# Optimization experiments

Measured on AMD Instinct MI355X. Metric: run time of the kernel, lower is better.

## Reference

```python
import jax, jax.numpy as jnp
import numpy as np

B, C, H, W = 16, 3, 1024, 1024
DENSITY = 0.015
SIGMA = 1.5
K = 5  # blur kernel size
N_FLAKES = int(H * W * DENSITY)  # 15728


def setup_inputs() -> dict:
    key = jax.random.key(0)
    kx, ky, kxs, kr = jax.random.split(key, 4)
    x = jax.random.uniform(kx, (B, C, H, W), dtype=jnp.float32)
    ys = jax.random.randint(ky, (B, N_FLAKES), 0, H, dtype=jnp.int32)
    xs = jax.random.randint(kxs, (B, N_FLAKES), 0, W, dtype=jnp.int32)
    rs = jax.random.randint(kr, (B, N_FLAKES), 1, 4, dtype=jnp.int32)  # radius in {1,2,3}
    return {"x": x, "ys": ys, "xs": xs, "rs": rs}


def reference(x, ys, xs, rs):
    Bb, Cc, Hh, Ww = x.shape
    # --- vectorized flake stamping (replaces per-flake Python loop) ---
    # Each flake writes a (2r+1)x(2r+1) square of 0.95, clipped to image bounds.
    # Max radius is 3 -> enumerate the 7x7 = 49 candidate offsets per flake.
    off = jnp.arange(-3, 4)
    dyg, dxg = jnp.meshgrid(off, off, indexing="ij")
    dy = dyg.reshape(-1)  # [49]
    dx = dxg.reshape(-1)  # [49]
    r = rs[..., None]  # [B, N, 1]
    valid = (jnp.abs(dy) <= r) & (jnp.abs(dx) <= r)  # [B, N, 49]
    # Clamping out-of-bounds coords to the border is equivalent to torch's
    # slice-clipping because the written value is a constant (0.95) and the
    # border pixel is already covered by an in-range offset. Invalid offsets
    # (|d| > r) are redirected to the flake center, which is always stamped.
    yy = jnp.where(valid, jnp.clip(ys[..., None] + dy, 0, Hh - 1), ys[..., None])
    xx = jnp.where(valid, jnp.clip(xs[..., None] + dx, 0, Ww - 1), xs[..., None])
    b = jnp.arange(Bb)[:, None, None]  # [B,1,1]
    out = x.at[b, :, yy, xx].set(0.95)  # stamp all channels

    # --- depthwise 5x5 gaussian blur ---
    coords = jnp.arange(K, dtype=jnp.float32) - K // 2
    g = jnp.exp(-(coords ** 2) / (2.0 * SIGMA ** 2))
    g = g / g.sum()
    kern = jnp.outer(g, g).astype(x.dtype)[None, None]  # [1,1,5,5]
    kern = jnp.broadcast_to(kern, (Cc, 1, K, K))  # depthwise: O=C, I=1
    pad = K // 2
    out = jax.lax.conv_general_dilated(
        out, kern, window_strides=(1, 1), padding=[(pad, pad), (pad, pad)],
        feature_group_count=Cc, dimension_numbers=("NCHW", "OIHW", "NCHW"))
    return jnp.clip(out, 0.0, 1.0)
```

## Files before the change

kernel.cpp:

```cpp
#include <hip/hip_runtime.h>


#define H_ 1024
#define W_ 1024
#define B_ 16
#define C_ 3
#define NF_ 15728
#define MASK_WORDS_PER_B (H_ * W_ / 32)

#define G0 0.12007838f
#define G1 0.23388076f
#define G2 0.29208172f

__global__ void clear_mask_kernel(uint4* __restrict__ mask, int n4) {
    int i = blockIdx.x * blockDim.x + threadIdx.x;
    if (i < n4) mask[i] = make_uint4(0u, 0u, 0u, 0u);
}

__global__ void stamp_kernel(const int* __restrict__ ys, const int* __restrict__ xs,
                             const int* __restrict__ rs, unsigned int* __restrict__ mask) {
    int t = blockIdx.x * blockDim.x + threadIdx.x;
    if (t >= B_ * NF_) return;
    int b = t / NF_;
    int y0 = ys[t], x0 = xs[t], r = rs[t];
    unsigned int* mb = mask + b * MASK_WORDS_PER_B;
    int xlo = max(x0 - r, 0), xhi = min(x0 + r, W_ - 1);
    int ylo = max(y0 - r, 0), yhi = min(y0 + r, H_ - 1);
    for (int y = ylo; y <= yhi; ++y) {
        int i0 = (y << 10) + xlo;
        int i1 = (y << 10) + xhi;
        int w0 = i0 >> 5, w1 = i1 >> 5;
        unsigned int m0 = ~0u << (i0 & 31);
        unsigned int m1 = ~0u >> (31 - (i1 & 31));
        if (w0 == w1) {
            atomicOr(mb + w0, m0 & m1);
        } else {
            atomicOr(mb + w0, m0);
            atomicOr(mb + w1, m1);
        }
    }
}

constexpr int TW = 128;
constexpr int TH = 32;

__global__ __launch_bounds__(256) void blur_kernel(const float* __restrict__ x,
                                                   const unsigned int* __restrict__ mask,
                                                   float* __restrict__ out) {
    int plane = blockIdx.z;
    int b = plane / C_;
    const float* xp = x + (size_t)plane * (H_ * W_);
    float* op = out + (size_t)plane * (H_ * W_);
    const unsigned int* mb = mask + b * MASK_WORDS_PER_B;

    const int tx0 = blockIdx.x * TW;
    const int ty0 = blockIdx.y * TH;
    const int tid = threadIdx.x;

    __shared__ float4 smid[TH][35];

    for (int i = tid; i < TH * 34; i += 256) {
        int r = i / 34;
        int j = i - 34 * r;
        int gx4 = tx0 - 4 + 4 * j;
        float4 acc = make_float4(0.f, 0.f, 0.f, 0.f);
        if ((unsigned)gx4 < (unsigned)W_) {
            int cw = gx4 >> 5;
            int bit = gx4 & 31;
            int gy0 = ty0 + r - 2;
            #pragma unroll
            for (int k = 0; k < 5; ++k) {
                const float wk = (k == 0 || k == 4) ? G0 : ((k == 1 || k == 3) ? G1 : G2);
                int gy = gy0 + k;
                if ((unsigned)gy < (unsigned)H_) {
                    float4 v = *(const float4*)(xp + (gy << 10) + gx4);
                    unsigned int mw = mb[(gy << 5) + cw];
                    if ((mw >> (bit + 0)) & 1u) v.x = 0.95f;
                    if ((mw >> (bit + 1)) & 1u) v.y = 0.95f;
                    if ((mw >> (bit + 2)) & 1u) v.z = 0.95f;
                    if ((mw >> (bit + 3)) & 1u) v.w = 0.95f;
                    acc.x += wk * v.x;
                    acc.y += wk * v.y;
                    acc.z += wk * v.z;
                    acc.w += wk * v.w;
                }
            }
        }
        smid[r][j] = acc;
    }
    __syncthreads();

    for (int i = tid; i < TH * 32; i += 256) {
        int rr = i >> 5;
        int j = i & 31;
        float2 A  = *(const float2*)((const float*)&smid[rr][j] + 2);
        float4 Bv = smid[rr][j + 1];
        float2 Cv = *(const float2*)((const float*)&smid[rr][j + 2]);
        float4 o;
        o.x = G0 * (A.x  + Bv.z) + G1 * (A.y  + Bv.y) + G2 * Bv.x;
        o.y = G0 * (A.y  + Bv.w) + G1 * (Bv.x + Bv.z) + G2 * Bv.y;
        o.z = G0 * (Bv.x + Cv.x) + G1 * (Bv.y + Bv.w) + G2 * Bv.z;
        o.w = G0 * (Bv.y + Cv.y) + G1 * (Bv.z + Cv.x) + G2 * Bv.w;
        o.x = fminf(fmaxf(o.x, 0.0f), 1.0f);
        o.y = fminf(fmaxf(o.y, 0.0f), 1.0f);
        o.z = fminf(fmaxf(o.z, 0.0f), 1.0f);
        o.w = fminf(fmaxf(o.w, 0.0f), 1.0f);
        *(float4*)(op + ((ty0 + rr) << 10) + tx0 + 4 * j) = o;
    }
}

extern "C" void kernel_launch(void* const* d_in, const int* in_sizes, int n_in,
                              void* d_out, int out_size, void* d_ws, size_t ws_size,
                              hipStream_t stream) {
    const float* x  = (const float*)d_in[0];
    const int*   ys = (const int*)d_in[1];
    const int*   xs = (const int*)d_in[2];
    const int*   rs = (const int*)d_in[3];
    float* out = (float*)d_out;
    unsigned int* mask = (unsigned int*)d_ws;

    int n4 = B_ * MASK_WORDS_PER_B / 4;
    clear_mask_kernel<<<dim3((n4 + 255) / 256), dim3(256), 0, stream>>>((uint4*)mask, n4);

    int nst = B_ * NF_;
    stamp_kernel<<<dim3((nst + 255) / 256), dim3(256), 0, stream>>>(ys, xs, rs, mask);

    dim3 grid(W_ / TW, H_ / TH, B_ * C_);
    blur_kernel<<<grid, dim3(256), 0, stream>>>(x, mask, out);
}
```

Measured before the change: 484.2 us.

## Stage raw masked tile with halo in LDS and do vertical blur from shared memory

The blur kernel used to compute the vertical 5-tap pass while loading, so every input row and mask word was read five times from global memory. Now the (TH+4)x136 masked input tile, halo included, is loaded once into shared memory, and both vertical and horizontal passes read from LDS. This cuts redundant global and L2 traffic in exchange for more LDS reads per output and a slightly larger shared buffer, with possible bank conflicts from the float2 reads at offset 8.

```diff
diff --git a/kernel.cpp b/kernel.cpp
--- a/kernel.cpp
+++ b/kernel.cpp
@@ -57,50 +57,50 @@
     const int ty0 = blockIdx.y * TH;
     const int tid = threadIdx.x;
 
-    __shared__ float4 smid[TH][35];
+    __shared__ float4 sin4[TH + 4][35];
 
-    for (int i = tid; i < TH * 34; i += 256) {
+    for (int i = tid; i < (TH + 4) * 34; i += 256) {
         int r = i / 34;
         int j = i - 34 * r;
+        int gy = ty0 + r - 2;
         int gx4 = tx0 - 4 + 4 * j;
-        float4 acc = make_float4(0.f, 0.f, 0.f, 0.f);
-        if ((unsigned)gx4 < (unsigned)W_) {
-            int cw = gx4 >> 5;
+        float4 v = make_float4(0.f, 0.f, 0.f, 0.f);
+        if ((unsigned)gy < (unsigned)H_ && (unsigned)gx4 < (unsigned)W_) {
+            v = *(const float4*)(xp + (gy << 10) + gx4);
+            unsigned int mw = mb[(gy << 5) + (gx4 >> 5)];
             int bit = gx4 & 31;
-            int gy0 = ty0 + r - 2;
-            #pragma unroll
-            for (int k = 0; k < 5; ++k) {
-                const float wk = (k == 0 || k == 4) ? G0 : ((k == 1 || k == 3) ? G1 : G2);
-                int gy = gy0 + k;
-                if ((unsigned)gy < (unsigned)H_) {
-                    float4 v = *(const float4*)(xp + (gy << 10) + gx4);
-                    unsigned int mw = mb[(gy << 5) + cw];
-                    if ((mw >> (bit + 0)) & 1u) v.x = 0.95f;
-                    if ((mw >> (bit + 1)) & 1u) v.y = 0.95f;
-                    if ((mw >> (bit + 2)) & 1u) v.z = 0.95f;
-                    if ((mw >> (bit + 3)) & 1u) v.w = 0.95f;
-                    acc.x += wk * v.x;
-                    acc.y += wk * v.y;
-                    acc.z += wk * v.z;
-                    acc.w += wk * v.w;
-                }
-            }
+            if ((mw >> (bit + 0)) & 1u) v.x = 0.95f;
+            if ((mw >> (bit + 1)) & 1u) v.y = 0.95f;
+            if ((mw >> (bit + 2)) & 1u) v.z = 0.95f;
+            if ((mw >> (bit + 3)) & 1u) v.w = 0.95f;
         }
-        smid[r][j] = acc;
+        sin4[r][j] = v;
     }
     __syncthreads();
 
     for (int i = tid; i < TH * 32; i += 256) {
         int rr = i >> 5;
         int j = i & 31;
-        float2 A  = *(const float2*)((const float*)&smid[rr][j] + 2);
-        float4 Bv = smid[rr][j + 1];
-        float2 Cv = *(const float2*)((const float*)&smid[rr][j + 2]);
+        float2 va = make_float2(0.f, 0.f);
+        float4 vb = make_float4(0.f, 0.f, 0.f, 0.f);
+        float2 vc = make_float2(0.f, 0.f);
+        #pragma unroll
+        for (int k = 0; k < 5; ++k) {
+            const float wk = (k == 0 || k == 4) ? G0 : ((k == 1 || k == 3) ? G1 : G2);
+            const float* row = (const float*)&sin4[rr + k][j];
+            float2 a  = *(const float2*)(row + 2);
+            float4 bv = *(const float4*)(row + 4);
+            float2 cv = *(const float2*)(row + 8);
+            va.x += wk * a.x;  va.y += wk * a.y;
+            vb.x += wk * bv.x; vb.y += wk * bv.y;
+            vb.z += wk * bv.z; vb.w += wk * bv.w;
+            vc.x += wk * cv.x; vc.y += wk * cv.y;
+        }
         float4 o;
-        o.x = G0 * (A.x  + Bv.z) + G1 * (A.y  + Bv.y) + G2 * Bv.x;
-        o.y = G0 * (A.y  + Bv.w) + G1 * (Bv.x + Bv.z) + G2 * Bv.y;
-        o.z = G0 * (Bv.x + Cv.x) + G1 * (Bv.y + Bv.w) + G2 * Bv.z;
-        o.w = G0 * (Bv.y + Cv.y) + G1 * (Bv.z + Cv.x) + G2 * Bv.w;
+        o.x = G0 * (va.x + vb.z) + G1 * (va.y + vb.y) + G2 * vb.x;
+        o.y = G0 * (va.y + vb.w) + G1 * (vb.x + vb.z) + G2 * vb.y;
+        o.z = G0 * (vb.x + vc.x) + G1 * (vb.y + vb.w) + G2 * vb.z;
+        o.w = G0 * (vb.y + vc.y) + G1 * (vb.z + vc.x) + G2 * vb.w;
         o.x = fminf(fmaxf(o.x, 0.0f), 1.0f);
         o.y = fminf(fmaxf(o.y, 0.0f), 1.0f);
         o.z = fminf(fmaxf(o.z, 0.0f), 1.0f);
```

Measured after the change: 403.8 us. 16.6% less time.

## Stream rows through registers with rolling vertical accumulators and shuffle-based horizontal pass

Applied to the files above, without the earlier changes.

Replaces the shared-memory two-pass tiled blur with a per-band streaming kernel. Each block covers a full row width and 32 rows. Each thread keeps five rolling vertical accumulators in registers and prefetches the next rows. The horizontal pass uses warp shuffles with edge-lane halo loads instead of LDS, which removes the 5x redundant vertical reads and the block sync. It risks lower parallelism per block and higher register pressure from the fully unrolled loop.

```diff
diff --git a/kernel.cpp b/kernel.cpp
--- a/kernel.cpp
+++ b/kernel.cpp
@@ -41,71 +41,113 @@
     }
 }
 
-constexpr int TW = 128;
-constexpr int TH = 32;
+constexpr int BAND = 32;
+constexpr int NITER = BAND + 4;
 
-__global__ __launch_bounds__(256) void blur_kernel(const float* __restrict__ x,
-                                                   const unsigned int* __restrict__ mask,
-                                                   float* __restrict__ out) {
-    int plane = blockIdx.z;
-    int b = plane / C_;
+__global__ __launch_bounds__(256, 4) void blur_kernel(const float* __restrict__ x,
+                                                      const unsigned int* __restrict__ mask,
+                                                      float* __restrict__ out) {
+    const int plane = blockIdx.z;
+    const int b = plane / C_;
     const float* xp = x + (size_t)plane * (H_ * W_);
     float* op = out + (size_t)plane * (H_ * W_);
     const unsigned int* mb = mask + b * MASK_WORDS_PER_B;
 
-    const int tx0 = blockIdx.x * TW;
-    const int ty0 = blockIdx.y * TH;
     const int tid = threadIdx.x;
+    const int wv = tid >> 6;
+    const int ln = tid & 63;
+    const int gx4 = (wv << 8) + (ln << 2);
+    const int y0 = blockIdx.y * BAND;
 
-    __shared__ float4 smid[TH][35];
+    const bool isL = (ln == 0), isR = (ln == 63);
+    const int hoff = isL ? gx4 - 2 : gx4 + 4;
+    const bool haloOn = (isL || isR) && ((unsigned)hoff < (unsigned)W_);
+    const int mwi = gx4 >> 5, mbit = gx4 & 31;
+    const int hwi = hoff >> 5, hbit = hoff & 31;
 
-    for (int i = tid; i < TH * 34; i += 256) {
-        int r = i / 34;
-        int j = i - 34 * r;
-        int gx4 = tx0 - 4 + 4 * j;
-        float4 acc = make_float4(0.f, 0.f, 0.f, 0.f);
-        if ((unsigned)gx4 < (unsigned)W_) {
-            int cw = gx4 >> 5;
-            int bit = gx4 & 31;
-            int gy0 = ty0 + r - 2;
-            #pragma unroll
-            for (int k = 0; k < 5; ++k) {
-                const float wk = (k == 0 || k == 4) ? G0 : ((k == 1 || k == 3) ? G1 : G2);
-                int gy = gy0 + k;
-                if ((unsigned)gy < (unsigned)H_) {
-                    float4 v = *(const float4*)(xp + (gy << 10) + gx4);
-                    unsigned int mw = mb[(gy << 5) + cw];
-                    if ((mw >> (bit + 0)) & 1u) v.x = 0.95f;
-                    if ((mw >> (bit + 1)) & 1u) v.y = 0.95f;
-                    if ((mw >> (bit + 2)) & 1u) v.z = 0.95f;
-                    if ((mw >> (bit + 3)) & 1u) v.w = 0.95f;
-                    acc.x += wk * v.x;
-                    acc.y += wk * v.y;
-                    acc.z += wk * v.z;
-                    acc.w += wk * v.w;
-                }
-            }
+    float4 acc[5];
+    float2 hacc[5];
+    #pragma unroll
+    for (int s = 0; s < 5; ++s) {
+        acc[s] = make_float4(0.f, 0.f, 0.f, 0.f);
+        hacc[s] = make_float2(0.f, 0.f);
+    }
+
+    float4 px[2];  unsigned int pm[2];
+    float2 ph[2];  unsigned int phm[2];
+    px[0] = px[1] = make_float4(0.f, 0.f, 0.f, 0.f);
+    ph[0] = ph[1] = make_float2(0.f, 0.f);
+    pm[0] = pm[1] = 0u; phm[0] = phm[1] = 0u;
+
+    auto load_row = [&](int i, float4& vx, unsigned int& vm,
+                        float2& vh, unsigned int& vhm) {
+        int gy = y0 - 2 + i;
+        if ((unsigned)gy < (unsigned)H_) {
+            vx = *(const float4*)(xp + (gy << 10) + gx4);
+            vm = mb[(gy << 5) + mwi];
+            if (haloOn) {
+                vh = *(const float2*)(xp + (gy << 10) + hoff);
+                vhm = mb[(gy << 5) + hwi];
+            } else { vh = make_float2(0.f, 0.f); vhm = 0u; }
+        } else {
+            vx = make_float4(0.f, 0.f, 0.f, 0.f); vm = 0u;
+            vh = make_float2(0.f, 0.f); vhm = 0u;
         }
-        smid[r][j] = acc;
-    }
-    __syncthreads();
+    };
 
-    for (int i = tid; i < TH * 32; i += 256) {
-        int rr = i >> 5;
-        int j = i & 31;
-        float2 A  = *(const float2*)((const float*)&smid[rr][j] + 2);
-        float4 Bv = smid[rr][j + 1];
-        float2 Cv = *(const float2*)((const float*)&smid[rr][j + 2]);
-        float4 o;
-        o.x = G0 * (A.x  + Bv.z) + G1 * (A.y  + Bv.y) + G2 * Bv.x;
-        o.y = G0 * (A.y  + Bv.w) + G1 * (Bv.x + Bv.z) + G2 * Bv.y;
-        o.z = G0 * (Bv.x + Cv.x) + G1 * (Bv.y + Bv.w) + G2 * Bv.z;
-        o.w = G0 * (Bv.y + Cv.y) + G1 * (Bv.z + Cv.x) + G2 * Bv.w;
-        o.x = fminf(fmaxf(o.x, 0.0f), 1.0f);
-        o.y = fminf(fmaxf(o.y, 0.0f), 1.0f);
-        o.z = fminf(fmaxf(o.z, 0.0f), 1.0f);
-        o.w = fminf(fmaxf(o.w, 0.0f), 1.0f);
-        *(float4*)(op + ((ty0 + rr) << 10) + tx0 + 4 * j) = o;
+    load_row(0, px[0], pm[0], ph[0], phm[0]);
+    load_row(1, px[1], pm[1], ph[1], phm[1]);
+
+    #pragma unroll
+    for (int i = 0; i < NITER; ++i) {
+        float4 vr = px[i & 1];
+        unsigned int m = pm[i & 1];
+        if ((m >> (mbit + 0)) & 1u) vr.x = 0.95f;
+        if ((m >> (mbit + 1)) & 1u) vr.y = 0.95f;
+        if ((m >> (mbit + 2)) & 1u) vr.z = 0.95f;
+        if ((m >> (mbit + 3)) & 1u) vr.w = 0.95f;
+        float2 hr = ph[i & 1];
+        unsigned int hm = phm[i & 1];
+        if ((hm >> (hbit + 0)) & 1u) hr.x = 0.95f;
+        if ((hm >> (hbit + 1)) & 1u) hr.y = 0.95f;
+
+        if (i + 2 < NITER) load_row(i + 2, px[i & 1], pm[i & 1], ph[i & 1], phm[i & 1]);
+
+        #pragma unroll
+        for (int d = -2; d <= 2; ++d) {
+            int ti = i - 2 + d;
+            if (ti < 0 || ti >= BAND) continue;
+            const float wk = (d == -2 || d == 2) ? G0 : ((d == -1 || d == 1) ? G1 : G2);
+            const int sl = ti % 5;
+            acc[sl].x += wk * vr.x; acc[sl].y += wk * vr.y;
+            acc[sl].z += wk * vr.z; acc[sl].w += wk * vr.w;
+            hacc[sl].x += wk * hr.x; hacc[sl].y += wk * hr.y;
+        }
+
+        if (i >= 4) {
+            const int ti = i - 4;
+            const int sl = ti % 5;
+            float4 vb = acc[sl];
+            float2 hvb = hacc[sl];
+            float az = __shfl_up(vb.z, 1u);
+            float aw = __shfl_up(vb.w, 1u);
+            float cx = __shfl_down(vb.x, 1u);
+            float cy = __shfl_down(vb.y, 1u);
+            az = isL ? hvb.x : az;  aw = isL ? hvb.y : aw;
+            cx = isR ? hvb.x : cx;  cy = isR ? hvb.y : cy;
+            float4 o;
+            o.x = G0 * (az + vb.z) + G1 * (aw + vb.y) + G2 * vb.x;
+            o.y = G0 * (aw + vb.w) + G1 * (vb.x + vb.z) + G2 * vb.y;
+            o.z = G0 * (vb.x + cx) + G1 * (vb.y + vb.w) + G2 * vb.z;
+            o.w = G0 * (vb.y + cy) + G1 * (vb.z + cx) + G2 * vb.w;
+            o.x = fminf(fmaxf(o.x, 0.0f), 1.0f);
+            o.y = fminf(fmaxf(o.y, 0.0f), 1.0f);
+            o.z = fminf(fmaxf(o.z, 0.0f), 1.0f);
+            o.w = fminf(fmaxf(o.w, 0.0f), 1.0f);
+            *(float4*)(op + ((y0 + ti) << 10) + gx4) = o;
+            acc[sl] = make_float4(0.f, 0.f, 0.f, 0.f);
+            hacc[sl] = make_float2(0.f, 0.f);
+        }
     }
 }
 
@@ -125,6 +167,6 @@
     int nst = B_ * NF_;
     stamp_kernel<<<dim3((nst + 255) / 256), dim3(256), 0, stream>>>(ys, xs, rs, mask);
 
-    dim3 grid(W_ / TW, H_ / TH, B_ * C_);
+    dim3 grid(1, H_ / BAND, B_ * C_);
     blur_kernel<<<grid, dim3(256), 0, stream>>>(x, mask, out);
 }
```

Result: faster. 423.3 us (-12.6%).
